# Performance work log

Hardware: AMD Instinct MI355X
Metric: run time of the kernel (lower is better)

## Reference

```python
import jax, jax.numpy as jnp
import numpy as np

# DeepSeek MLA prefill pipeline (absorbed form), matching the GEMM/bmm/sparse-attention
# Dims: m=512 tokens, hidden=7168, d_kv_c=512, d_q_c=1536, d_r=64, d_q=d_kv=128,
# h=16 local heads, attention dim d = d_kv_c + d_r = 576, s_kv=4096, topk=512.

M, HID = 512, 7168
D_KV_C, D_Q_C, D_R, D_Q, D_KV = 512, 1536, 64, 128, 128
H = 16
S_KV, TOPK = 4096, 512
D_ATT = D_KV_C + D_R  # 576


def setup_inputs() -> dict:
    key = jax.random.key(0)
    ks = jax.random.split(key, 8)
    s = lambda n: 1.0 / np.sqrt(n).astype(np.float32)
    return {
        "x": jax.random.normal(ks[0], (M, HID), jnp.float32),
        "W_cqkv": jax.random.normal(ks[1], (HID, D_KV_C + D_Q_C + D_R), jnp.float32) * s(HID),
        "W_uq": jax.random.normal(ks[2], (D_Q_C, H * (D_Q + D_R)), jnp.float32) * s(D_Q_C),
        "W_qk": jax.random.normal(ks[3], (H, D_Q, D_KV_C), jnp.float32) * s(D_Q),
        "kv_cache": jax.random.normal(ks[4], (S_KV, D_ATT), jnp.float32),
        "W_o1": jax.random.normal(ks[5], (H, D_KV_C, D_KV), jnp.float32) * s(D_KV_C),
        "W_oproj": jax.random.normal(ks[6], (H * D_KV, HID), jnp.float32) * s(H * D_KV),
        "indices": jax.random.randint(ks[7], (M, TOPK), 0, S_KV, jnp.int32),
    }


def reference(x, W_cqkv, W_uq, W_qk, kv_cache, W_o1, W_oproj, indices):
    # 1) QKV compression GEMM: [m, hid] @ [hid, d_kv_c + d_q_c + d_r]
    c = x @ W_cqkv
    kv_c_new = c[:, :D_KV_C]                      # compressed KV (would extend cache)
    q_c = c[:, D_KV_C:D_KV_C + D_Q_C]             # [m, d_q_c]
    # (kv_c_new / k_r_new feed the cache in a real pipeline; attention below reads

    # 2) Q uncompression GEMM: [m, d_q_c] @ [d_q_c, h*(d_q+d_r)]
    q = (q_c @ W_uq).reshape(M, H, D_Q + D_R)
    q_nope, q_pe = q[..., :D_Q], q[..., D_Q:]     # [m,h,128], [m,h,64]

    # 3) Q absorb bmm: per-head [m, d_q] @ [d_q, d_kv_c]
    q_abs = jnp.einsum('mhq,hqc->mhc', q_nope, W_qk)
    q_full = jnp.concatenate([q_abs, q_pe], axis=-1)  # [m, h, 576]

    # 4) Top-k sparse MLA attention (flash_mla_sparse_fwd math):
    #    indices shared across heads (h_kv = 1); gather kv rows per query token.
    kv_g = kv_cache[indices]                      # [m, topk, 576]
    sm_scale = 1.0 / jnp.sqrt(jnp.float32(D_ATT))
    scores = jnp.einsum('mhd,mtd->mht', q_full, kv_g) * sm_scale
    attn = jax.nn.softmax(scores, axis=-1)        # [m, h, topk]
    o = jnp.einsum('mht,mtc->mhc', attn, kv_g[..., :D_KV_C])  # value = first d_kv_c dims

    # 5) O bmm: per-head [m, d_kv_c] @ [d_kv_c, d_kv]
    o2 = jnp.einsum('mhc,hcv->mhv', o, W_o1)      # [m, h, 128]

    # 6) O projection GEMM: [m, h*d_kv] @ [h*d_kv, hid]
    out = o2.reshape(M, H * D_KV) @ W_oproj       # [m, hid]
    return out
```

## Files before the change

### kernel.cpp

```cpp
#include <hip/hip_runtime.h>
#include <hip/hip_bf16.h>

#define M_DIM 512
#define HID 7168
#define D_KV_C 512
#define D_Q_C 1536
#define D_R 64
#define D_Q 128
#define D_KV 128
#define H_DIM 16
#define S_KV 4096
#define TOPK 512
#define D_ATT 576
#define SPLIT 2
#define SROWS 256

typedef _Float16 half_t;
typedef __attribute__((ext_vector_type(8))) _Float16 f16x8_t;
typedef __attribute__((ext_vector_type(4))) float f32x4_t;
typedef __attribute__((ext_vector_type(2))) unsigned int u32x2_t;

#define MFMA_F16(a, b, c) __builtin_amdgcn_mfma_f32_16x16x32_f16((a), (b), (c), 0, 0, 0)

__device__ __forceinline__ unsigned lds_addr32(const void* p) {
    return (unsigned)(unsigned long long)(const __attribute__((address_space(3))) char*)p;
}

typedef const __attribute__((address_space(1))) unsigned int* gptr_t;
typedef __attribute__((address_space(3))) unsigned int* lptr_t;
__device__ __forceinline__ void gload_lds16(const void* g, void* l) {
    __builtin_amdgcn_global_load_lds((gptr_t)g, (lptr_t)l, 16, 0, 0);
}

__global__ __launch_bounds__(256) void cvt_f16(const float* __restrict__ src,
                                               half_t* __restrict__ dst, int n8)
{
    int i = blockIdx.x * 256 + threadIdx.x;
    if (i >= n8) return;
    const float4* s = (const float4*)src + (size_t)i * 2;
    float4 a = s[0], b = s[1];
    f16x8_t o;
    o[0] = (half_t)a.x; o[1] = (half_t)a.y; o[2] = (half_t)a.z; o[3] = (half_t)a.w;
    o[4] = (half_t)b.x; o[5] = (half_t)b.y; o[6] = (half_t)b.z; o[7] = (half_t)b.w;
    *(f16x8_t*)(dst + (size_t)i * 8) = o;
}

template<int NS>
__global__ __launch_bounds__(256) void cvt_sum(const float* __restrict__ src, long long slice,
                                               half_t* __restrict__ dst, int n8)
{
    int i = blockIdx.x * 256 + threadIdx.x;
    if (i >= n8) return;
    float a[8] = {};
    #pragma unroll
    for (int s = 0; s < NS; s++) {
        const float4* p = (const float4*)(src + (size_t)s * slice) + (size_t)i * 2;
        float4 u = p[0], v = p[1];
        a[0] += u.x; a[1] += u.y; a[2] += u.z; a[3] += u.w;
        a[4] += v.x; a[5] += v.y; a[6] += v.z; a[7] += v.w;
    }
    f16x8_t o;
    #pragma unroll
    for (int j = 0; j < 8; j++) o[j] = (half_t)a[j];
    *(f16x8_t*)(dst + (size_t)i * 8) = o;
}

__global__ __launch_bounds__(256) void cvt_sum_q(const float* __restrict__ src, long long slice,
                                                 half_t* __restrict__ q16, half_t* __restrict__ qf)
{
    int i = blockIdx.x * 256 + threadIdx.x;
    if (i >= M_DIM * 3072 / 8) return;
    float a[8] = {};
    #pragma unroll
    for (int s = 0; s < 2; s++) {
        const float4* p = (const float4*)(src + (size_t)s * slice) + (size_t)i * 2;
        float4 u = p[0], v = p[1];
        a[0] += u.x; a[1] += u.y; a[2] += u.z; a[3] += u.w;
        a[4] += v.x; a[5] += v.y; a[6] += v.z; a[7] += v.w;
    }
    f16x8_t o;
    #pragma unroll
    for (int j = 0; j < 8; j++) o[j] = (half_t)a[j];
    *(f16x8_t*)(q16 + (size_t)i * 8) = o;
    int col = (i * 8) % 3072;
    int c = col % 192;
    if (c >= 128) {
        int row = (i * 8) / 3072, h = col / 192;
        int mh = row * 16 + h;
        *(f16x8_t*)(qf + (size_t)mh * D_ATT + D_KV_C + (c - 128)) = o;
    }
}

__global__ __launch_bounds__(256) void cvt_t(
    const float* __restrict__ src, int ld_src, long long sS,
    half_t* __restrict__ dst, int ld_dst, long long sD)
{
    src += (size_t)blockIdx.z * sS;
    dst += (size_t)blockIdx.z * sD;
    int k0 = blockIdx.y * 64, n0 = blockIdx.x * 64;
    __shared__ half_t t[64][80];
    int tid = threadIdx.x;
    int kr = tid >> 4, nc = (tid & 15) * 4;
    #pragma unroll
    for (int i = 0; i < 4; i++) {
        float4 v = *(const float4*)&src[(size_t)(k0 + kr + i * 16) * ld_src + n0 + nc];
        t[nc + 0][kr + i * 16] = (half_t)v.x;
        t[nc + 1][kr + i * 16] = (half_t)v.y;
        t[nc + 2][kr + i * 16] = (half_t)v.z;
        t[nc + 3][kr + i * 16] = (half_t)v.w;
    }
    __syncthreads();
    int nr = tid >> 2, kc = (tid & 3) * 16;
    f16x8_t w0 = *(const f16x8_t*)&t[nr][kc];
    f16x8_t w1 = *(const f16x8_t*)&t[nr][kc + 8];
    *(f16x8_t*)&dst[(size_t)(n0 + nr) * ld_dst + k0 + kc] = w0;
    *(f16x8_t*)&dst[(size_t)(n0 + nr) * ld_dst + k0 + kc + 8] = w1;
}

template<bool F16OUT>
__global__ __launch_bounds__(256) void gemm_f16t(
    const half_t* __restrict__ A, int lda, long long sA,
    const half_t* __restrict__ Bt, int ldb, long long sB,
    void* __restrict__ Cv, int ldc, long long sC, int K)
{
    A  += (size_t)blockIdx.z * sA;
    Bt += (size_t)blockIdx.z * sB;
    const int bm = blockIdx.y * 64, bn = blockIdx.x * 64;

    __shared__ __align__(16) char lds[2][16384];

    const int tid = threadIdx.x, w = tid >> 6, lane = tid & 63;
    const int l15 = lane & 15, q = lane >> 4;
    const int wr = w >> 1, wc = w & 1;

    const half_t* gA[2];
    const half_t* gB[2];
    #pragma unroll
    for (int p = 0; p < 2; p++) {
        int c = p * 64 + lane;
        int rl = c >> 3;
        int sg = (c & 7) ^ (rl & 7);
        gA[p] = A  + (size_t)(bm + w * 16 + rl) * lda + sg * 8;
        gB[p] = Bt + (size_t)(bn + w * 16 + rl) * ldb + sg * 8;
    }

    f32x4_t acc[2][2];
    #pragma unroll
    for (int i = 0; i < 2; i++)
        #pragma unroll
        for (int j = 0; j < 2; j++) acc[i][j] = (f32x4_t){0.f, 0.f, 0.f, 0.f};

    const int nsteps = K >> 6;

    {
        char* ab = lds[0];
        char* bb = ab + 8192;
        #pragma unroll
        for (int p = 0; p < 2; p++) {
            gload_lds16(gA[p], ab + w * 2048 + p * 1024);
            gload_lds16(gB[p], bb + w * 2048 + p * 1024);
        }
    }
    __syncthreads();

    int cur = 0;
    for (int s = 0; s < nsteps; s++) {
        if (s + 1 < nsteps) {
            int k0 = (s + 1) << 6;
            char* ab = lds[cur ^ 1];
            char* bb = ab + 8192;
            #pragma unroll
            for (int p = 0; p < 2; p++) {
                gload_lds16(gA[p] + k0, ab + w * 2048 + p * 1024);
                gload_lds16(gB[p] + k0, bb + w * 2048 + p * 1024);
            }
        }
        {
            const char* ab = lds[cur];
            const char* bb = ab + 8192;
            #pragma unroll
            for (int kk = 0; kk < 2; kk++) {
                f16x8_t av[2], bv[2];
                #pragma unroll
                for (int i = 0; i < 2; i++) {
                    int ra = wr * 32 + i * 16 + l15;
                    av[i] = *(const f16x8_t*)(ab + ra * 128 + (((kk * 4 + q) ^ (ra & 7)) * 16));
                    int rb = wc * 32 + i * 16 + l15;
                    bv[i] = *(const f16x8_t*)(bb + rb * 128 + (((kk * 4 + q) ^ (rb & 7)) * 16));
                }
                #pragma unroll
                for (int i = 0; i < 2; i++)
                    #pragma unroll
                    for (int j = 0; j < 2; j++)
                        acc[i][j] = MFMA_F16(av[i], bv[j], acc[i][j]);
            }
        }
        __syncthreads();
        cur ^= 1;
    }

    half_t* Ch = (half_t*)Cv + (F16OUT ? (size_t)blockIdx.z * sC : 0);
    float*  Cf = (float*)Cv  + (F16OUT ? 0 : (size_t)blockIdx.z * sC);
    #pragma unroll
    for (int i = 0; i < 2; i++)
        #pragma unroll
        for (int j = 0; j < 2; j++)
            #pragma unroll
            for (int r = 0; r < 4; r++) {
                size_t row = bm + wr * 32 + i * 16 + q * 4 + r;
                size_t col = bn + wc * 32 + j * 16 + l15;
                if (F16OUT) Ch[row * ldc + col] = (half_t)acc[i][j][r];
                else        Cf[row * ldc + col] = acc[i][j][r];
            }
}

__global__ __launch_bounds__(512) void attn_split(
    const half_t* __restrict__ qf,
    const half_t* __restrict__ kvb,
    const int* __restrict__ indices,
    half_t* __restrict__ op,
    float2* __restrict__ ml)
{
    const int m = blockIdx.x, sp = blockIdx.y;
    const int tid = threadIdx.x;
    const int w = tid >> 6, lane = tid & 63;
    const int l15 = lane & 15, q = lane >> 4;

    __shared__ __align__(16) char u_mem[32768];
    __shared__ __align__(16) unsigned short p_s[16 * SROWS];

    float* s_s = (float*)u_mem;
    unsigned short* v_s = (unsigned short*)u_mem;

    const int* idxp = indices + (size_t)m * TOPK + sp * SROWS;

    int rows[2];
    rows[0] = idxp[(w * 2 + 0) * 16 + l15];
    rows[1] = idxp[(w * 2 + 1) * 16 + l15];

    f32x4_t acc[2];
    acc[0] = (f32x4_t){0.f, 0.f, 0.f, 0.f};
    acc[1] = (f32x4_t){0.f, 0.f, 0.f, 0.f};

    const half_t* qh = qf + ((size_t)m * 16 + l15) * D_ATT + q * 8;

    #pragma unroll 3
    for (int kk = 0; kk < 18; kk++) {
        f16x8_t ah = *(const f16x8_t*)(qh + kk * 32);
        #pragma unroll
        for (int tt = 0; tt < 2; tt++) {
            f16x8_t b = *(const f16x8_t*)(kvb + (size_t)rows[tt] * D_ATT + kk * 32 + q * 8);
            acc[tt] = MFMA_F16(ah, b, acc[tt]);
        }
    }

    const float scale = 1.0f / 24.0f;
    #pragma unroll
    for (int tt = 0; tt < 2; tt++) {
        int t = (w * 2 + tt) * 16 + l15;
        #pragma unroll
        for (int r = 0; r < 4; r++)
            s_s[(q * 4 + r) * 260 + t] = acc[tt][r] * scale;
    }
    __syncthreads();

    {
        int h = tid >> 5, j = tid & 31;
        float mx = -1e30f;
        #pragma unroll
        for (int t = j; t < SROWS; t += 32) mx = fmaxf(mx, s_s[h * 260 + t]);
        #pragma unroll
        for (int off = 16; off; off >>= 1) mx = fmaxf(mx, __shfl_xor(mx, off, 32));
        float sum = 0.f;
        #pragma unroll
        for (int t = j; t < SROWS; t += 32) {
            float e = __expf(s_s[h * 260 + t] - mx);
            sum += e;
            union { half_t hh; unsigned short u; } cv;
            cv.hh = (half_t)e;
            unsigned byte = ((unsigned)(t * 2)) ^ (((unsigned)(h & 7)) << 4);
            p_s[h * SROWS + (byte >> 1)] = cv.u;
        }
        #pragma unroll
        for (int off = 16; off; off >>= 1) sum += __shfl_xor(sum, off, 32);
        if (j == 0)
            ml[(size_t)sp * (M_DIM * H_DIM) + m * 16 + h] = make_float2(mx, sum);
    }
    __syncthreads();

    f32x4_t oacc[4];
    #pragma unroll
    for (int i = 0; i < 4; i++) oacc[i] = (f32x4_t){0.f, 0.f, 0.f, 0.f};

    const unsigned vbase = lds_addr32(v_s);
    const int trow = tid >> 4, jb4 = tid & 15;
    const unsigned swz_w = (((unsigned)(trow & 7)) << 4) ^ (((unsigned)((trow >> 3) & 3)) << 5);

    int rstage[8];
    #pragma unroll
    for (int ct = 0; ct < 8; ct++) rstage[ct] = idxp[ct * 32 + trow];

    const int row1 = q * 8 + (l15 >> 2);
    const int row2 = row1 + 4;
    const unsigned sw1 = (((unsigned)(row1 & 7)) << 4) ^ (((unsigned)q & 3u) << 5);
    const unsigned sw2 = (((unsigned)(row2 & 7)) << 4) ^ (((unsigned)q & 3u) << 5);
    const unsigned cbyte = (unsigned)((l15 & 3) * 8);

    #pragma unroll 1
    for (int ct = 0; ct < 8; ct++) {
        {
            const half_t* src = kvb + (size_t)rstage[ct] * D_ATT + jb4 * 32;
            f16x8_t tmp[4];
            #pragma unroll
            for (int i = 0; i < 4; i++) tmp[i] = *(const f16x8_t*)(src + i * 8);
            #pragma unroll
            for (int i = 0; i < 4; i++) {
                unsigned byte = ((unsigned)(jb4 * 64 + i * 16)) ^ swz_w;
                *(f16x8_t*)((char*)v_s + trow * 1024 + byte) = tmp[i];
            }
        }
        __syncthreads();

        f16x8_t pa;
        {
            unsigned pbyte = ((unsigned)(ct * 64 + q * 16)) ^ (((unsigned)(l15 & 7)) << 4);
            pa = *(const f16x8_t*)((const char*)p_s + l15 * (SROWS * 2) + pbyte);
        }

        u32x2_t blo[4], bhi[4];
        #pragma unroll
        for (int i = 0; i < 4; i++) {
            unsigned c2 = ((unsigned)((w * 4 + i) * 32)) + cbyte;
            unsigned a1 = vbase + (unsigned)row1 * 1024u + (c2 ^ sw1);
            unsigned a2 = vbase + (unsigned)row2 * 1024u + (c2 ^ sw2);
            asm volatile("ds_read_b64_tr_b16 %0, %1 offset:0" : "=v"(blo[i]) : "v"(a1) : "memory");
            asm volatile("ds_read_b64_tr_b16 %0, %1 offset:0" : "=v"(bhi[i]) : "v"(a2) : "memory");
        }
        asm volatile("s_waitcnt lgkmcnt(0)" ::: "memory");
        __builtin_amdgcn_sched_barrier(0);

        __builtin_amdgcn_s_setprio(1);
        #pragma unroll
        for (int i = 0; i < 4; i++) {
            union { f16x8_t s; struct { u32x2_t lo, hi; } u; } f;
            f.u.lo = blo[i]; f.u.hi = bhi[i];
            oacc[i] = MFMA_F16(pa, f.s, oacc[i]);
        }
        __builtin_amdgcn_s_setprio(0);

        __syncthreads();
    }

    half_t* ob = op + ((size_t)sp * M_DIM + m) * (H_DIM * D_KV_C);
    #pragma unroll
    for (int i = 0; i < 4; i++) {
        int c = (w * 4 + i) * 16 + l15;
        #pragma unroll
        for (int r = 0; r < 4; r++)
            ob[(size_t)(q * 4 + r) * D_KV_C + c] = (half_t)oacc[i][r];
    }
}

__global__ __launch_bounds__(256) void attn_merge(
    const half_t* __restrict__ op,
    const float2* __restrict__ ml,
    half_t* __restrict__ o)
{
    int idx = blockIdx.x * 256 + threadIdx.x;
    if (idx >= M_DIM * H_DIM * D_KV_C / 8) return;
    int mh = idx >> 6;
    int c8 = (idx & 63) * 8;
    float2 a = ml[mh];
    float2 b = ml[M_DIM * H_DIM + mh];
    float Mx = fmaxf(a.x, b.x);
    float w0 = __expf(a.x - Mx), w1 = __expf(b.x - Mx);
    float inv = 1.0f / (w0 * a.y + w1 * b.y);
    w0 *= inv; w1 *= inv;
    f16x8_t v0 = *(const f16x8_t*)(op + (size_t)mh * D_KV_C + c8);
    f16x8_t v1 = *(const f16x8_t*)(op + ((size_t)(M_DIM * H_DIM) + mh) * D_KV_C + c8);
    f16x8_t o8;
    #pragma unroll
    for (int j = 0; j < 8; j++)
        o8[j] = (half_t)(w0 * (float)v0[j] + w1 * (float)v1[j]);
    *(f16x8_t*)(o + (size_t)mh * D_KV_C + c8) = o8;
}

extern "C" void kernel_launch(void* const* d_in, const int* in_sizes, int n_in,
                              void* d_out, int out_size, void* d_ws, size_t ws_size,
                              hipStream_t stream)
{
    const float* x        = (const float*)d_in[0];
    const float* W_cqkv   = (const float*)d_in[1];
    const float* W_uq     = (const float*)d_in[2];
    const float* W_qk     = (const float*)d_in[3];
    const float* kv_cache = (const float*)d_in[4];
    const float* W_o1     = (const float*)d_in[5];
    const float* W_oproj  = (const float*)d_in[6];
    const int*   indices  = (const int*)d_in[7];
    float* out = (float*)d_out;

    half_t* wsh = (half_t*)d_ws;
    half_t* Wcqkv_t = wsh;
    half_t* qc16    = wsh;
    half_t* o_part  = wsh;
    half_t* q32h    = wsh + 786432;
    half_t* q16     = wsh + 7077888;
    half_t* x16     = wsh + 11010048;
    half_t* o2_16   = wsh + 11010048;
    half_t* Wuq_t   = wsh + 14680064;
    half_t* o16     = wsh + 14680064;
    half_t* Wqk_t   = wsh + 19398656;
    half_t* ml_h    = wsh + 19398656;
    half_t* Wo1_t   = wsh + 20447232;
    half_t* Wop_t   = wsh + 21495808;
    half_t* kv16    = wsh + 36175872;
    half_t* qc32h   = wsh + 38535168;
    half_t* qf16    = wsh + 38535168;
    float*  qc32 = (float*)qc32h;
    float*  q32  = (float*)q32h;
    float2* ml   = (float2*)ml_h;


    cvt_f16<<<(M_DIM * HID / 8 + 255) / 256, 256, 0, stream>>>(x, x16, M_DIM * HID / 8);
    cvt_f16<<<(S_KV * D_ATT / 8 + 255) / 256, 256, 0, stream>>>(kv_cache, kv16, S_KV * D_ATT / 8);
    cvt_t<<<dim3(D_Q_C / 64, HID / 64, 1), 256, 0, stream>>>(
        W_cqkv + D_KV_C, D_KV_C + D_Q_C + D_R, 0, Wcqkv_t, HID, 0);
    cvt_t<<<dim3(3072 / 64, D_Q_C / 64, 1), 256, 0, stream>>>(
        W_uq, 3072, 0, Wuq_t, D_Q_C, 0);
    cvt_t<<<dim3(D_KV_C / 64, D_Q / 64, H_DIM), 256, 0, stream>>>(
        W_qk, D_KV_C, D_Q * D_KV_C, Wqk_t, D_Q, D_Q * D_KV_C);
    cvt_t<<<dim3(D_KV / 64, D_KV_C / 64, H_DIM), 256, 0, stream>>>(
        W_o1, D_KV, D_KV_C * D_KV, Wo1_t, D_KV_C, D_KV_C * D_KV);
    cvt_t<<<dim3(HID / 64, 2048 / 64, 1), 256, 0, stream>>>(
        W_oproj, HID, 0, Wop_t, 2048, 0);

    gemm_f16t<false><<<dim3(D_Q_C / 64, M_DIM / 64, 4), 256, 0, stream>>>(
        x16, HID, 1792, Wcqkv_t, HID, 1792, qc32, D_Q_C, (long long)M_DIM * D_Q_C, 1792);
    cvt_sum<4><<<(M_DIM * D_Q_C / 8 + 255) / 256, 256, 0, stream>>>(
        qc32, (long long)M_DIM * D_Q_C, qc16, M_DIM * D_Q_C / 8);

    gemm_f16t<false><<<dim3(3072 / 64, M_DIM / 64, 2), 256, 0, stream>>>(
        qc16, D_Q_C, 768, Wuq_t, D_Q_C, 768, q32, 3072, (long long)M_DIM * 3072, 768);
    cvt_sum_q<<<(M_DIM * 3072 / 8 + 255) / 256, 256, 0, stream>>>(
        q32, (long long)M_DIM * 3072, q16, qf16);

    gemm_f16t<true><<<dim3(D_KV_C / 64, M_DIM / 64, H_DIM), 256, 0, stream>>>(
        q16, 3072, D_Q + D_R, Wqk_t, D_Q, (long long)D_Q * D_KV_C,
        qf16, H_DIM * D_ATT, D_ATT, D_Q);

    attn_split<<<dim3(M_DIM, SPLIT), 512, 0, stream>>>(qf16, kv16, indices, o_part, ml);
    attn_merge<<<(M_DIM * H_DIM * D_KV_C / 8 + 255) / 256, 256, 0, stream>>>(o_part, ml, o16);

    gemm_f16t<true><<<dim3(D_KV / 64, M_DIM / 64, H_DIM), 256, 0, stream>>>(
        o16, H_DIM * D_KV_C, D_KV_C, Wo1_t, D_KV_C, (long long)D_KV_C * D_KV,
        o2_16, H_DIM * D_KV, D_KV, D_KV_C);

    gemm_f16t<false><<<dim3(HID / 64, M_DIM / 64, 1), 256, 0, stream>>>(
        o2_16, H_DIM * D_KV, 0, Wop_t, 2048, 0, out, HID, 0, H_DIM * D_KV);
}
```

Baseline: 222.8 us.

## Restructure sparse attention: async double-buffered V loads, register softmax, prescaled Q

Reworks the attention kernel so gathered KV rows for the value phase are loaded straight into LDS with global_load_lds into a double buffer, prefetching the next chunk while the current one is consumed. This replaces the register-staged copy and one barrier per chunk. Softmax is now done in registers with cross-wave reductions through small LDS arrays, replacing the score round-trip through shared memory. The softmax scale is folded into the Q-absorb GEMM epilogue and the q_pe copy. It also adds an occupancy hint and doubles the LDS buffer, which may reduce blocks per CU.

```diff
diff --git a/kernel.cpp b/kernel.cpp
--- a/kernel.cpp
+++ b/kernel.cpp
@@ -14,6 +14,7 @@
 #define D_ATT 576
 #define SPLIT 2
 #define SROWS 256
+#define SM_SCALE (1.0f / 24.0f)
 
 typedef _Float16 half_t;
 typedef __attribute__((ext_vector_type(8))) _Float16 f16x8_t;
@@ -87,7 +88,10 @@
     if (c >= 128) {
         int row = (i * 8) / 3072, h = col / 192;
         int mh = row * 16 + h;
-        *(f16x8_t*)(qf + (size_t)mh * D_ATT + D_KV_C + (c - 128)) = o;
+        f16x8_t os;
+        #pragma unroll
+        for (int j = 0; j < 8; j++) os[j] = (half_t)(a[j] * SM_SCALE);
+        *(f16x8_t*)(qf + (size_t)mh * D_ATT + D_KV_C + (c - 128)) = os;
     }
 }
 
@@ -121,7 +125,7 @@
 __global__ __launch_bounds__(256) void gemm_f16t(
     const half_t* __restrict__ A, int lda, long long sA,
     const half_t* __restrict__ Bt, int ldb, long long sB,
-    void* __restrict__ Cv, int ldc, long long sC, int K)
+    void* __restrict__ Cv, int ldc, long long sC, int K, float alpha)
 {
     A  += (size_t)blockIdx.z * sA;
     Bt += (size_t)blockIdx.z * sB;
@@ -209,12 +213,13 @@
             for (int r = 0; r < 4; r++) {
                 size_t row = bm + wr * 32 + i * 16 + q * 4 + r;
                 size_t col = bn + wc * 32 + j * 16 + l15;
-                if (F16OUT) Ch[row * ldc + col] = (half_t)acc[i][j][r];
-                else        Cf[row * ldc + col] = acc[i][j][r];
+                float v = acc[i][j][r] * alpha;
+                if (F16OUT) Ch[row * ldc + col] = (half_t)v;
+                else        Cf[row * ldc + col] = v;
             }
 }
 
-__global__ __launch_bounds__(512) void attn_split(
+__global__ __launch_bounds__(512, 4) void attn_split(
     const half_t* __restrict__ qf,
     const half_t* __restrict__ kvb,
     const int* __restrict__ indices,
@@ -226,100 +231,113 @@
     const int w = tid >> 6, lane = tid & 63;
     const int l15 = lane & 15, q = lane >> 4;
 
-    __shared__ __align__(16) char u_mem[32768];
+    __shared__ __align__(16) char vbuf[2][32768];
     __shared__ __align__(16) unsigned short p_s[16 * SROWS];
-
-    float* s_s = (float*)u_mem;
-    unsigned short* v_s = (unsigned short*)u_mem;
+    __shared__ float red_m[16][8];
+    __shared__ float red_s[16][8];
 
     const int* idxp = indices + (size_t)m * TOPK + sp * SROWS;
 
-    int rows[2];
-    rows[0] = idxp[(w * 2 + 0) * 16 + l15];
-    rows[1] = idxp[(w * 2 + 1) * 16 + l15];
-
-    f32x4_t acc[2];
-    acc[0] = (f32x4_t){0.f, 0.f, 0.f, 0.f};
-    acc[1] = (f32x4_t){0.f, 0.f, 0.f, 0.f};
-
-    const half_t* qh = qf + ((size_t)m * 16 + l15) * D_ATT + q * 8;
-
-    #pragma unroll 3
+    {
+        #pragma unroll
+        for (int j = 0; j < 4; j++) {
+            int R = 4 * w + j;
+            int grow = idxp[R];
+            unsigned swz = (((unsigned)(R & 7)) << 4) ^ (((unsigned)((R >> 3) & 3)) << 5);
+            const char* src = (const char*)(kvb + (size_t)grow * D_ATT) + (((unsigned)(16 * lane)) ^ swz);
+            gload_lds16(src, vbuf[0] + R * 1024);
+        }
+    }
+
+    const int rows0 = idxp[(w * 2 + 0) * 16 + l15];
+    const int rows1 = idxp[(w * 2 + 1) * 16 + l15];
+
+    f32x4_t acc0 = (f32x4_t){0.f, 0.f, 0.f, 0.f};
+    f32x4_t acc1 = (f32x4_t){0.f, 0.f, 0.f, 0.f};
+
+    const half_t* qp  = qf  + ((size_t)m * 16 + l15) * D_ATT + q * 8;
+    const half_t* kp0 = kvb + (size_t)rows0 * D_ATT + q * 8;
+    const half_t* kp1 = kvb + (size_t)rows1 * D_ATT + q * 8;
+
+    #pragma unroll
     for (int kk = 0; kk < 18; kk++) {
-        f16x8_t ah = *(const f16x8_t*)(qh + kk * 32);
-        #pragma unroll
-        for (int tt = 0; tt < 2; tt++) {
-            f16x8_t b = *(const f16x8_t*)(kvb + (size_t)rows[tt] * D_ATT + kk * 32 + q * 8);
-            acc[tt] = MFMA_F16(ah, b, acc[tt]);
-        }
-    }
-
-    const float scale = 1.0f / 24.0f;
-    #pragma unroll
-    for (int tt = 0; tt < 2; tt++) {
-        int t = (w * 2 + tt) * 16 + l15;
-        #pragma unroll
-        for (int r = 0; r < 4; r++)
-            s_s[(q * 4 + r) * 260 + t] = acc[tt][r] * scale;
+        f16x8_t ah = *(const f16x8_t*)(qp  + kk * 32);
+        f16x8_t b0 = *(const f16x8_t*)(kp0 + kk * 32);
+        f16x8_t b1 = *(const f16x8_t*)(kp1 + kk * 32);
+        acc0 = MFMA_F16(ah, b0, acc0);
+        acc1 = MFMA_F16(ah, b1, acc1);
+    }
+
+    float gm[4], e0[4], e1[4];
+    #pragma unroll
+    for (int r = 0; r < 4; r++) {
+        float mx = fmaxf(acc0[r], acc1[r]);
+        #pragma unroll
+        for (int off = 8; off; off >>= 1) mx = fmaxf(mx, __shfl_xor(mx, off, 16));
+        if (l15 == 0) red_m[q * 4 + r][w] = mx;
     }
     __syncthreads();
-
-    {
-        int h = tid >> 5, j = tid & 31;
-        float mx = -1e30f;
-        #pragma unroll
-        for (int t = j; t < SROWS; t += 32) mx = fmaxf(mx, s_s[h * 260 + t]);
-        #pragma unroll
-        for (int off = 16; off; off >>= 1) mx = fmaxf(mx, __shfl_xor(mx, off, 32));
-        float sum = 0.f;
-        #pragma unroll
-        for (int t = j; t < SROWS; t += 32) {
-            float e = __expf(s_s[h * 260 + t] - mx);
-            sum += e;
-            union { half_t hh; unsigned short u; } cv;
-            cv.hh = (half_t)e;
-            unsigned byte = ((unsigned)(t * 2)) ^ (((unsigned)(h & 7)) << 4);
-            p_s[h * SROWS + (byte >> 1)] = cv.u;
-        }
-        #pragma unroll
-        for (int off = 16; off; off >>= 1) sum += __shfl_xor(sum, off, 32);
-        if (j == 0)
-            ml[(size_t)sp * (M_DIM * H_DIM) + m * 16 + h] = make_float2(mx, sum);
+    #pragma unroll
+    for (int r = 0; r < 4; r++) {
+        int h = q * 4 + r;
+        float mx = red_m[h][0];
+        #pragma unroll
+        for (int ww = 1; ww < 8; ww++) mx = fmaxf(mx, red_m[h][ww]);
+        gm[r] = mx;
+        e0[r] = __expf(acc0[r] - mx);
+        e1[r] = __expf(acc1[r] - mx);
+        float s = e0[r] + e1[r];
+        #pragma unroll
+        for (int off = 8; off; off >>= 1) s += __shfl_xor(s, off, 16);
+        if (l15 == 0) red_s[h][w] = s;
     }
     __syncthreads();
+    if (w == 0 && l15 == 0) {
+        #pragma unroll
+        for (int r = 0; r < 4; r++) {
+            int h = q * 4 + r;
+            float s = 0.f;
+            #pragma unroll
+            for (int ww = 0; ww < 8; ww++) s += red_s[h][ww];
+            ml[(size_t)sp * (M_DIM * H_DIM) + m * 16 + h] = make_float2(gm[r], s);
+        }
+    }
+    #pragma unroll
+    for (int r = 0; r < 4; r++) {
+        int h = q * 4 + r;
+        int t0 = (w * 2 + 0) * 16 + l15;
+        int t1 = t0 + 16;
+        union { half_t hh; unsigned short u; } c0, c1;
+        c0.hh = (half_t)e0[r]; c1.hh = (half_t)e1[r];
+        p_s[h * SROWS + ((((unsigned)(t0 * 2)) ^ (((unsigned)(h & 7)) << 4)) >> 1)] = c0.u;
+        p_s[h * SROWS + ((((unsigned)(t1 * 2)) ^ (((unsigned)(h & 7)) << 4)) >> 1)] = c1.u;
+    }
+    __syncthreads();
 
     f32x4_t oacc[4];
     #pragma unroll
     for (int i = 0; i < 4; i++) oacc[i] = (f32x4_t){0.f, 0.f, 0.f, 0.f};
-
-    const unsigned vbase = lds_addr32(v_s);
-    const int trow = tid >> 4, jb4 = tid & 15;
-    const unsigned swz_w = (((unsigned)(trow & 7)) << 4) ^ (((unsigned)((trow >> 3) & 3)) << 5);
-
-    int rstage[8];
-    #pragma unroll
-    for (int ct = 0; ct < 8; ct++) rstage[ct] = idxp[ct * 32 + trow];
 
     const int row1 = q * 8 + (l15 >> 2);
     const int row2 = row1 + 4;
-    const unsigned sw1 = (((unsigned)(row1 & 7)) << 4) ^ (((unsigned)q & 3u) << 5);
-    const unsigned sw2 = (((unsigned)(row2 & 7)) << 4) ^ (((unsigned)q & 3u) << 5);
+    const unsigned sw1 = (((unsigned)(row1 & 7)) << 4) ^ (((unsigned)((row1 >> 3) & 3)) << 5);
+    const unsigned sw2 = (((unsigned)(row2 & 7)) << 4) ^ (((unsigned)((row2 >> 3) & 3)) << 5);
     const unsigned cbyte = (unsigned)((l15 & 3) * 8);
 
     #pragma unroll 1
     for (int ct = 0; ct < 8; ct++) {
-        {
-            const half_t* src = kvb + (size_t)rstage[ct] * D_ATT + jb4 * 32;
-            f16x8_t tmp[4];
+        if (ct < 7) {
             #pragma unroll
-            for (int i = 0; i < 4; i++) tmp[i] = *(const f16x8_t*)(src + i * 8);
-            #pragma unroll
-            for (int i = 0; i < 4; i++) {
-                unsigned byte = ((unsigned)(jb4 * 64 + i * 16)) ^ swz_w;
-                *(f16x8_t*)((char*)v_s + trow * 1024 + byte) = tmp[i];
+            for (int j = 0; j < 4; j++) {
+                int R = 4 * w + j;
+                int grow = idxp[(ct + 1) * 32 + R];
+                unsigned swz = (((unsigned)(R & 7)) << 4) ^ (((unsigned)((R >> 3) & 3)) << 5);
+                const char* src = (const char*)(kvb + (size_t)grow * D_ATT) + (((unsigned)(16 * lane)) ^ swz);
+                gload_lds16(src, vbuf[(ct + 1) & 1] + R * 1024);
             }
         }
-        __syncthreads();
+
+        const unsigned vb = lds_addr32(vbuf[ct & 1]);
 
         f16x8_t pa;
         {
@@ -331,8 +349,8 @@
         #pragma unroll
         for (int i = 0; i < 4; i++) {
             unsigned c2 = ((unsigned)((w * 4 + i) * 32)) + cbyte;
-            unsigned a1 = vbase + (unsigned)row1 * 1024u + (c2 ^ sw1);
-            unsigned a2 = vbase + (unsigned)row2 * 1024u + (c2 ^ sw2);
+            unsigned a1 = vb + (unsigned)row1 * 1024u + (c2 ^ sw1);
+            unsigned a2 = vb + (unsigned)row2 * 1024u + (c2 ^ sw2);
             asm volatile("ds_read_b64_tr_b16 %0, %1 offset:0" : "=v"(blo[i]) : "v"(a1) : "memory");
             asm volatile("ds_read_b64_tr_b16 %0, %1 offset:0" : "=v"(bhi[i]) : "v"(a2) : "memory");
         }
@@ -420,7 +438,6 @@
     float*  q32  = (float*)q32h;
     float2* ml   = (float2*)ml_h;
 
-
     cvt_f16<<<(M_DIM * HID / 8 + 255) / 256, 256, 0, stream>>>(x, x16, M_DIM * HID / 8);
     cvt_f16<<<(S_KV * D_ATT / 8 + 255) / 256, 256, 0, stream>>>(kv_cache, kv16, S_KV * D_ATT / 8);
     cvt_t<<<dim3(D_Q_C / 64, HID / 64, 1), 256, 0, stream>>>(
@@ -435,26 +452,26 @@
         W_oproj, HID, 0, Wop_t, 2048, 0);
 
     gemm_f16t<false><<<dim3(D_Q_C / 64, M_DIM / 64, 4), 256, 0, stream>>>(
-        x16, HID, 1792, Wcqkv_t, HID, 1792, qc32, D_Q_C, (long long)M_DIM * D_Q_C, 1792);
+        x16, HID, 1792, Wcqkv_t, HID, 1792, qc32, D_Q_C, (long long)M_DIM * D_Q_C, 1792, 1.0f);
     cvt_sum<4><<<(M_DIM * D_Q_C / 8 + 255) / 256, 256, 0, stream>>>(
         qc32, (long long)M_DIM * D_Q_C, qc16, M_DIM * D_Q_C / 8);
 
     gemm_f16t<false><<<dim3(3072 / 64, M_DIM / 64, 2), 256, 0, stream>>>(
-        qc16, D_Q_C, 768, Wuq_t, D_Q_C, 768, q32, 3072, (long long)M_DIM * 3072, 768);
+        qc16, D_Q_C, 768, Wuq_t, D_Q_C, 768, q32, 3072, (long long)M_DIM * 3072, 768, 1.0f);
     cvt_sum_q<<<(M_DIM * 3072 / 8 + 255) / 256, 256, 0, stream>>>(
         q32, (long long)M_DIM * 3072, q16, qf16);
 
     gemm_f16t<true><<<dim3(D_KV_C / 64, M_DIM / 64, H_DIM), 256, 0, stream>>>(
         q16, 3072, D_Q + D_R, Wqk_t, D_Q, (long long)D_Q * D_KV_C,
-        qf16, H_DIM * D_ATT, D_ATT, D_Q);
+        qf16, H_DIM * D_ATT, D_ATT, D_Q, SM_SCALE);
 
     attn_split<<<dim3(M_DIM, SPLIT), 512, 0, stream>>>(qf16, kv16, indices, o_part, ml);
     attn_merge<<<(M_DIM * H_DIM * D_KV_C / 8 + 255) / 256, 256, 0, stream>>>(o_part, ml, o16);
 
     gemm_f16t<true><<<dim3(D_KV / 64, M_DIM / 64, H_DIM), 256, 0, stream>>>(
         o16, H_DIM * D_KV_C, D_KV_C, Wo1_t, D_KV_C, (long long)D_KV_C * D_KV,
-        o2_16, H_DIM * D_KV, D_KV, D_KV_C);
+        o2_16, H_DIM * D_KV, D_KV, D_KV_C, 1.0f);
 
     gemm_f16t<false><<<dim3(HID / 64, M_DIM / 64, 1), 256, 0, stream>>>(
-        o2_16, H_DIM * D_KV, 0, Wop_t, 2048, 0, out, HID, 0, H_DIM * D_KV);
-}
+        o2_16, H_DIM * D_KV, 0, Wop_t, 2048, 0, out, HID, 0, 2048, 1.0f);
+}
```

New measurement: 215.9 us. -3.1%, faster.
